# Kernel optimization log

Hardware: AMD Instinct MI355X
Metric: run time of the kernel (lower is better)

## Reference

```python
import jax, jax.numpy as jnp
import numpy as np

N = 100_000   # num_nodes
D = 64        # emb_dim
E = 1_600_000 # num edges (before self loops)
L = 3         # n_layers
NEG_SLOPE = 0.2


def setup_inputs() -> dict:
    key = jax.random.key(0)
    ks = jax.random.split(key, 6)
    edge_index = jax.random.randint(ks[0], (2, E), 0, N, dtype=jnp.int32)
    # xavier-ish init for embedding and per-layer GATConv params
    emb = jax.random.normal(ks[1], (N, D), jnp.float32) * (1.0 / np.sqrt(D))
    W = jax.random.normal(ks[2], (L, D, D), jnp.float32) * (1.0 / np.sqrt(D))
    att_src = jax.random.normal(ks[3], (L, D), jnp.float32) * 0.1
    att_dst = jax.random.normal(ks[4], (L, D), jnp.float32) * 0.1
    bias = jnp.zeros((L, D), jnp.float32)
    return {"edge_index": edge_index, "emb": emb, "W": W,
            "att_src": att_src, "att_dst": att_dst, "bias": bias}


def _gat_layer(x, src, dst, W, a_s, a_d, b):
    # PyG GATConv, heads=1, concat=False, self-loops already in (src, dst)
    h = x @ W                                   # [N, D]
    e_s = h @ a_s                               # [N] per-node src score
    e_d = h @ a_d                               # [N] per-node dst score
    e = jax.nn.leaky_relu(e_s[src] + e_d[dst], NEG_SLOPE)   # [E']
    # segment softmax grouped by destination node (max is detached in PyG)
    m = jax.lax.stop_gradient(jax.ops.segment_max(e, dst, num_segments=N))
    ex = jnp.exp(e - m[dst])
    denom = jax.ops.segment_sum(ex, dst, num_segments=N)
    alpha = ex / (denom[dst] + 1e-16)           # [E']
    out = jax.ops.segment_sum(alpha[:, None] * h[src], dst, num_segments=N)
    return out + b


def reference(edge_index, emb, W, att_src, att_dst, bias):
    loops = jnp.arange(N, dtype=edge_index.dtype)
    src = jnp.concatenate([edge_index[0], loops])
    dst = jnp.concatenate([edge_index[1], loops])
    x = emb
    outs = [x]
    for l in range(L):
        x = jax.nn.elu(_gat_layer(x, src, dst, W[l], att_src[l], att_dst[l], bias[l]))
        outs.append(x)
    return jnp.mean(jnp.stack(outs, axis=0), axis=0)  # [N, D]
```

## Files before the change

### kernel.cpp

```cpp
#include <hip/hip_runtime.h>
#include <hip/hip_bf16.h>


#define BSHIFT 9
#define NPB 512
#define COL_CAP 10240
#define FRAG_STRIDE 5120

typedef _Float16 v8h __attribute__((ext_vector_type(8)));
typedef float v4f __attribute__((ext_vector_type(4)));
typedef unsigned short u16x8 __attribute__((ext_vector_type(8)));

__device__ inline float bf2f(unsigned short u) {
    return __uint_as_float(((unsigned int)u) << 16);
}
__device__ inline unsigned short f2bf(float v) {
    __hip_bfloat16 b = __float2bfloat16(v);
    return *reinterpret_cast<unsigned short*>(&b);
}
__device__ inline unsigned short f2h_u(float v) {
    return __builtin_bit_cast(unsigned short, (_Float16)v);
}
__device__ inline float h2f_u(unsigned short u) {
    return (float)__builtin_bit_cast(_Float16, u);
}

__global__ __launch_bounds__(256) void detect_bf16_k(const unsigned int* raw, int* flag, int* ghist) {
    __shared__ int sc;
    if (threadIdx.x == 0) sc = 0;
    ghist[threadIdx.x] = 0;
    __syncthreads();
    int c = 0;
    for (int i = threadIdx.x; i < 4096; i += 256) {
        unsigned int b = (raw[i] >> 8) & 0x7Fu;
        if (b >= 0x3Bu && b <= 0x3Fu) c++;
    }
    atomicAdd(&sc, c);
    __syncthreads();
    if (threadIdx.x == 0) *flag = (sc > 2048) ? 1 : 0;
}

__device__ inline float load_in(const void* p, int i, int isbf) {
    if (isbf) return bf2f(((const unsigned short*)p)[i]);
    return ((const float*)p)[i];
}

__global__ __launch_bounds__(256) void conv_emb_k(const void* emb, unsigned short* x0,
                                                  int n, const int* flag) {
    int i = blockIdx.x * 256 + threadIdx.x;
    if (i >= n) return;
    x0[i] = f2h_u(load_in(emb, i, *flag));
}

__global__ __launch_bounds__(256) void conv_params_k(const void* W, const void* as_, const void* ad_,
                                                     const void* b_, unsigned short* Whf, float* bf,
                                                     int L_, const int* flag) {
    int i = blockIdx.x * 256 + threadIdx.x;
    int isbf = *flag;
    if (i < L_ * 4096) {
        int l = i >> 12, rem = i & 4095;
        int k = rem >> 6, c64 = rem & 63;
        int t = c64 >> 4, c = c64 & 15;
        int kf = k >> 5, quad = (k >> 3) & 3, j = k & 7;
        int f = t * 2 + kf, lane = quad * 16 + c;
        Whf[l * FRAG_STRIDE + (f * 64 + lane) * 8 + j] = f2h_u(load_in(W, i, isbf));
    }
    if (i < L_ * 1024) {
        int l = i >> 10, r = i & 1023;
        int kf = r >> 9, rr = r & 511;
        int lane = rr >> 3, j = rr & 7;
        int c = lane & 15, quad = lane >> 4;
        int k = kf * 32 + quad * 8 + j;
        float val = 0.f;
        if (c < 2) {
            const void* av = c ? ad_ : as_;
            float dot = 0.f;
            for (int cc = 0; cc < 64; ++cc)
                dot += load_in(W, l * 4096 + k * 64 + cc, isbf) * load_in(av, l * 64 + cc, isbf);
            val = dot;
        }
        Whf[l * FRAG_STRIDE + ((8 + kf) * 64 + lane) * 8 + j] = f2h_u(val);
    }
    if (i < L_ * 64) bf[i] = load_in(b_, i, isbf);
}


__global__ __launch_bounds__(256) void hist_k(const int* dst, int* ghist, int E) {
    __shared__ int h[256];
    h[threadIdx.x] = 0;
    __syncthreads();
    int cs = blockIdx.x * 4096;
    int ce = min(cs + 4096, E);
    for (int i = cs + threadIdx.x; i < ce; i += 256)
        atomicAdd(&h[dst[i] >> BSHIFT], 1);
    __syncthreads();
    if (h[threadIdx.x]) atomicAdd(&ghist[threadIdx.x], h[threadIdx.x]);
}

__global__ __launch_bounds__(256) void scan_nb_k(const int* ghist, int* pairs_base, int* col_base,
                                                 int* cursor, int* rowptr, int N, int E, int NB) {
    __shared__ int s1[256], s2[256];
    int t = threadIdx.x;
    int hv = (t < NB) ? ghist[t] : 0;
    int npb = (t < NB) ? min(N - (t << BSHIFT), NPB) : 0;
    s1[t] = hv; s2[t] = hv + npb;
    __syncthreads();
    for (int off = 1; off < 256; off <<= 1) {
        int t1 = (t >= off) ? s1[t - off] : 0;
        int t2 = (t >= off) ? s2[t - off] : 0;
        __syncthreads();
        s1[t] += t1; s2[t] += t2;
        __syncthreads();
    }
    if (t < NB) {
        pairs_base[t] = s1[t] - hv;
        cursor[t]     = s1[t] - hv;
        col_base[t]   = s2[t] - (hv + npb);
    }
    if (t == 0) rowptr[N] = E + N;
}

__global__ __launch_bounds__(256) void partition_k(const int* __restrict__ src,
                                                   const int* __restrict__ dst,
                                                   int* cursor, uint2* __restrict__ pairs,
                                                   int E, int NB) {
    __shared__ int cnt[256], base[256], rk[256];
    int t = threadIdx.x;
    cnt[t] = 0; rk[t] = 0;
    __syncthreads();
    int cs = blockIdx.x * 4096;
    int ce = min(cs + 4096, E);
    for (int i = cs + t; i < ce; i += 256)
        atomicAdd(&cnt[dst[i] >> BSHIFT], 1);
    __syncthreads();
    if (t < NB && cnt[t]) base[t] = atomicAdd(&cursor[t], cnt[t]);
    __syncthreads();
    for (int i = cs + t; i < ce; i += 256) {
        int d = dst[i];
        int b = d >> BSHIFT;
        int r = atomicAdd(&rk[b], 1);
        pairs[base[b] + r] = make_uint2((unsigned)src[i], (unsigned)d);
    }
}

__global__ __launch_bounds__(512) void build_k(const uint2* __restrict__ pairs,
                                               const int* __restrict__ ghist,
                                               const int* __restrict__ pairs_base,
                                               const int* __restrict__ col_base,
                                               int* __restrict__ rowptr, int* __restrict__ col,
                                               int N) {
    __shared__ int cnt[512], cnt2[512], sc[512], off[513];
    __shared__ int col_lds[COL_CAP];
    int b = blockIdx.x, t = threadIdx.x;
    int nloc = min(N - (b << BSHIFT), NPB);
    int ne = ghist[b], pb = pairs_base[b], cb = col_base[b];
    cnt[t] = 0; cnt2[t] = 0;
    __syncthreads();
    for (int i = t; i < ne; i += 512)
        atomicAdd(&cnt[pairs[pb + i].y & (NPB - 1)], 1);
    __syncthreads();
    int v = cnt[t] + (t < nloc ? 1 : 0);
    sc[t] = v;
    __syncthreads();
    for (int o = 1; o < 512; o <<= 1) {
        int tv = (t >= o) ? sc[t - o] : 0;
        __syncthreads();
        sc[t] += tv;
        __syncthreads();
    }
    off[t + 1] = sc[t];
    if (t == 0) off[0] = 0;
    __syncthreads();
    if (t < nloc) rowptr[(b << BSHIFT) + t] = cb + off[t];
    int total = off[nloc];
    bool fit = (total <= COL_CAP);
    for (int i = t; i < ne; i += 512) {
        uint2 p = pairs[pb + i];
        int loc = p.y & (NPB - 1);
        int pos = off[loc] + atomicAdd(&cnt2[loc], 1);
        if (fit) col_lds[pos] = (int)p.x;
        else     col[cb + pos] = (int)p.x;
    }
    if (t < nloc) {
        int pos = off[t + 1] - 1;
        int sv = (b << BSHIFT) + t;
        if (fit) col_lds[pos] = sv;
        else     col[cb + pos] = sv;
    }
    __syncthreads();
    if (fit)
        for (int i = t; i < total; i += 512) col[cb + i] = col_lds[i];
}


__global__ __launch_bounds__(256) void gemm_k(const unsigned short* __restrict__ x,
                                              const unsigned short* __restrict__ Whf,
                                              unsigned short* __restrict__ h,
                                              float* __restrict__ es, float* __restrict__ ed,
                                              int n, int nblk, int nwaves) {
    int lane = threadIdx.x & 63;
    int gwave = (blockIdx.x * 256 + threadIdx.x) >> 6;
    int c = lane & 15, quad = lane >> 4;

    v8h bfr[10];
    #pragma unroll
    for (int f = 0; f < 10; ++f)
        bfr[f] = *(const v8h*)(Whf + (size_t)(f * 64 + lane) * 8);

    v4f z = {0.f, 0.f, 0.f, 0.f};
    for (int nb = gwave; nb < nblk; nb += nwaves) {
        int base = nb * 16;
        int m = base + c; if (m >= n) m = n - 1;
        const v8h a0 = *(const v8h*)(x + (size_t)m * 64 + quad * 8);
        const v8h a1 = *(const v8h*)(x + (size_t)m * 64 + 32 + quad * 8);
        v4f acc[5];
        #pragma unroll
        for (int t = 0; t < 5; ++t) {
            acc[t] = __builtin_amdgcn_mfma_f32_16x16x32_f16(a0, bfr[2 * t], z, 0, 0, 0);
            acc[t] = __builtin_amdgcn_mfma_f32_16x16x32_f16(a1, bfr[2 * t + 1], acc[t], 0, 0, 0);
        }
        #pragma unroll
        for (int r = 0; r < 4; ++r) {
            int row = base + quad * 4 + r;
            if (row < n) {
                #pragma unroll
                for (int t = 0; t < 4; ++t)
                    h[(size_t)row * 64 + t * 16 + c] = f2h_u(acc[t][r]);
                if (c == 0) es[row] = acc[4][r];
                if (c == 1) ed[row] = acc[4][r];
            }
        }
    }
}

__device__ inline float elu_f(float v) { return v > 0.f ? v : (__expf(v) - 1.f); }

__global__ __launch_bounds__(256) void agg_k(const unsigned short* __restrict__ h,
                                             const float* __restrict__ es,
                                             const float* __restrict__ ed, const int* __restrict__ rowptr,
                                             const int* __restrict__ col, const float* __restrict__ bias,
                                             unsigned short* __restrict__ xo, int n) {
    int gw = (blockIdx.x * 256 + threadIdx.x) >> 6;
    int lane = threadIdx.x & 63;
    if (gw >= n) return;
    int start = rowptr[gw], end = rowptr[gw + 1];
    int deg = end - start;
    float edd = ed[gw];

    if (deg <= 64) {
        int c = 0;
        float e = -1e30f;
        if (lane < deg) {
            c = col[start + lane];
            float t = es[c] + edd;
            e = t > 0.f ? t : 0.2f * t;
        }
        float m = e;
        #pragma unroll
        for (int off = 32; off; off >>= 1) m = fmaxf(m, __shfl_xor(m, off));
        float ex = (lane < deg) ? __expf(e - m) : 0.f;
        float sum = ex;
        #pragma unroll
        for (int off = 32; off; off >>= 1) sum += __shfl_xor(sum, off);
        float a = ex / (sum + 1e-16f);

        int g = lane >> 3, j = lane & 7;
        float acc[8];
        #pragma unroll
        for (int i = 0; i < 8; ++i) acc[i] = 0.f;
        for (int t = 0; t < deg; t += 16) {
            int i0 = t + g, i1 = t + 8 + g;
            int   s0  = __shfl(c, i0), s1 = __shfl(c, i1);
            float al0 = __shfl(a, i0), al1 = __shfl(a, i1);
            bool p0 = i0 < deg, p1 = i1 < deg;
            u16x8 hv0, hv1;
            if (p0) hv0 = *(const u16x8*)(h + (size_t)s0 * 64 + j * 8);
            if (p1) hv1 = *(const u16x8*)(h + (size_t)s1 * 64 + j * 8);
            if (p0) {
                #pragma unroll
                for (int i = 0; i < 8; ++i) acc[i] = fmaf(al0, h2f_u(hv0[i]), acc[i]);
            }
            if (p1) {
                #pragma unroll
                for (int i = 0; i < 8; ++i) acc[i] = fmaf(al1, h2f_u(hv1[i]), acc[i]);
            }
        }
        #pragma unroll
        for (int off = 8; off < 64; off <<= 1)
            #pragma unroll
            for (int i = 0; i < 8; ++i)
                acc[i] += __shfl_xor(acc[i], off);

        if (g == 0) {
            u16x8 o;
            #pragma unroll
            for (int i = 0; i < 8; ++i)
                o[i] = f2h_u(elu_f(acc[i] + bias[j * 8 + i]));
            *(u16x8*)(xo + (size_t)gw * 64 + j * 8) = o;
        }
    } else {
        float m = -1e30f;
        for (int k = start + lane; k < end; k += 64) {
            float e = es[col[k]] + edd;
            e = e > 0.f ? e : 0.2f * e;
            m = fmaxf(m, e);
        }
        #pragma unroll
        for (int off = 32; off; off >>= 1) m = fmaxf(m, __shfl_xor(m, off));
        float sum = 0.f;
        for (int k = start + lane; k < end; k += 64) {
            float e = es[col[k]] + edd;
            e = e > 0.f ? e : 0.2f * e;
            sum += __expf(e - m);
        }
        #pragma unroll
        for (int off = 32; off; off >>= 1) sum += __shfl_xor(sum, off);
        float inv = 1.f / (sum + 1e-16f);
        float acc = 0.f;
        for (int k = start; k < end; ++k) {
            int s = col[k];
            float e = es[s] + edd;
            e = e > 0.f ? e : 0.2f * e;
            float al = __expf(e - m) * inv;
            acc = fmaf(al, h2f_u(h[(size_t)s * 64 + lane]), acc);
        }
        xo[(size_t)gw * 64 + lane] = f2h_u(elu_f(acc + bias[lane]));
    }
}

__global__ __launch_bounds__(256) void finalize_k(const unsigned short* __restrict__ x0,
                                                  const unsigned short* __restrict__ x1,
                                                  const unsigned short* __restrict__ x2,
                                                  const unsigned short* __restrict__ x3,
                                                  void* __restrict__ out, const int* flag, int n8) {
    int i = blockIdx.x * 256 + threadIdx.x;
    if (i >= n8) return;
    size_t base = (size_t)i * 8;
    u16x8 a = *(const u16x8*)(x0 + base);
    u16x8 b = *(const u16x8*)(x1 + base);
    u16x8 c = *(const u16x8*)(x2 + base);
    u16x8 d = *(const u16x8*)(x3 + base);
    float v[8];
    #pragma unroll
    for (int k = 0; k < 8; ++k)
        v[k] = (h2f_u(a[k]) + h2f_u(b[k]) + h2f_u(c[k]) + h2f_u(d[k])) * 0.25f;
    if (*flag) {
        u16x8 o;
        #pragma unroll
        for (int k = 0; k < 8; ++k) o[k] = f2bf(v[k]);
        *(u16x8*)((unsigned short*)out + base) = o;
    } else {
        float4 o0 = make_float4(v[0], v[1], v[2], v[3]);
        float4 o1 = make_float4(v[4], v[5], v[6], v[7]);
        *(float4*)((float*)out + base) = o0;
        *(float4*)((float*)out + base + 4) = o1;
    }
}


extern "C" void kernel_launch(void* const* d_in, const int* in_sizes, int n_in,
                              void* d_out, int out_size, void* d_ws, size_t ws_size,
                              hipStream_t stream) {
    const int*  edge = (const int*)d_in[0];
    const void* emb  = d_in[1];
    const void* W    = d_in[2];
    const void* as_  = d_in[3];
    const void* ad_  = d_in[4];
    const void* b_   = d_in[5];

    const int E = in_sizes[0] / 2;
    const int N = in_sizes[1] / 64;
    const int L = in_sizes[2] / 4096;
    const int NB = (N + NPB - 1) >> BSHIFT;
    const size_t N64 = (size_t)N * 64;

    char* p = (char*)d_ws;
    auto take = [&](size_t bytes) { char* r = p; p += (bytes + 255) & ~(size_t)255; return r; };
    unsigned short* x0 = (unsigned short*)take(N64 * 2);
    unsigned short* x1 = (unsigned short*)take(N64 * 2);
    unsigned short* x3 = (unsigned short*)take(N64 * 2);
    unsigned short* h  = (unsigned short*)take(N64 * 2);
    uint2* pairs   = (uint2*)take((size_t)E * 8 > N64 * 2 ? (size_t)E * 8 : N64 * 2);
    unsigned short* x2 = (unsigned short*)pairs;
    float* es      = (float*)take((size_t)N * 4);
    float* ed      = (float*)take((size_t)N * 4);
    unsigned short* Whf = (unsigned short*)take((size_t)L * FRAG_STRIDE * 2);
    float* bf      = (float*)take((size_t)L * 64 * 4);
    int* rowptr    = (int*)take((size_t)(N + 1) * 4);
    int* col       = (int*)take((size_t)(E + N) * 4);
    int* ghist     = (int*)take(256 * 4);
    int* pairs_base= (int*)take(256 * 4);
    int* col_base  = (int*)take(256 * 4);
    int* cursor    = (int*)take(256 * 4);
    int* flag      = (int*)take(4);

    const int* srcp = edge;
    const int* dstp = edge + E;
    int nchunk = (E + 4095) / 4096;

    detect_bf16_k<<<1, 256, 0, stream>>>((const unsigned int*)emb, flag, ghist);
    conv_emb_k<<<(int)((N64 + 255) / 256), 256, 0, stream>>>(emb, x0, (int)N64, flag);
    conv_params_k<<<(L * 4096 + 255) / 256, 256, 0, stream>>>(W, as_, ad_, b_, Whf, bf, L, flag);

    hist_k<<<nchunk, 256, 0, stream>>>(dstp, ghist, E);
    scan_nb_k<<<1, 256, 0, stream>>>(ghist, pairs_base, col_base, cursor, rowptr, N, E, NB);
    partition_k<<<nchunk, 256, 0, stream>>>(srcp, dstp, cursor, pairs, E, NB);
    build_k<<<NB, 512, 0, stream>>>(pairs, ghist, pairs_base, col_base, rowptr, col, N);

    const int nblk = (N + 15) / 16;
    const int ggrid = 512;
    unsigned short* xs[4] = {x0, x1, x2, x3};
    for (int l = 0; l < L; ++l) {
        gemm_k<<<ggrid, 256, 0, stream>>>(xs[l], Whf + (size_t)l * FRAG_STRIDE,
                                          h, es, ed, N, nblk, ggrid * 4);
        agg_k<<<(N + 3) / 4, 256, 0, stream>>>(h, es, ed, rowptr, col, bf + l * 64, xs[l + 1], N);
    }
    finalize_k<<<(int)((N64 / 8 + 255) / 256), 256, 0, stream>>>(x0, x1, x2, x3, d_out, flag,
                                                                 (int)(N64 / 8));
}
```

Before: 375.2 us.

## Fuse finalize into last aggregation, merge conversions, deterministic partition scan

Folds the layer-mean finalize into the last aggregation kernel so the final layer output is never written and reread. Merges the embedding and parameter conversion kernels into one launch. Replaces the atomic cursor partitioning with per-chunk histograms plus a per-bucket scan, so partition_k no longer recounts its chunk or issues global atomics. This adds one scan kernel and a histogram buffer that is read twice.

Measured after the change: 353.8 us. -5.7%, faster.

```diff
diff --git a/kernel.cpp b/kernel.cpp
--- a/kernel.cpp
+++ b/kernel.cpp
@@ -6,6 +6,7 @@
 #define NPB 512
 #define COL_CAP 10240
 #define FRAG_STRIDE 5120
+#define CHUNK 4096
 
 typedef _Float16 v8h __attribute__((ext_vector_type(8)));
 typedef float v4f __attribute__((ext_vector_type(4)));
@@ -25,10 +26,9 @@
     return (float)__builtin_bit_cast(_Float16, u);
 }
 
-__global__ __launch_bounds__(256) void detect_bf16_k(const unsigned int* raw, int* flag, int* ghist) {
+__global__ __launch_bounds__(256) void detect_bf16_k(const unsigned int* raw, int* flag) {
     __shared__ int sc;
     if (threadIdx.x == 0) sc = 0;
-    ghist[threadIdx.x] = 0;
     __syncthreads();
     int c = 0;
     for (int i = threadIdx.x; i < 4096; i += 256) {
@@ -45,18 +45,13 @@
     return ((const float*)p)[i];
 }
 
-__global__ __launch_bounds__(256) void conv_emb_k(const void* emb, unsigned short* x0,
-                                                  int n, const int* flag) {
-    int i = blockIdx.x * 256 + threadIdx.x;
-    if (i >= n) return;
-    x0[i] = f2h_u(load_in(emb, i, *flag));
-}
-
-__global__ __launch_bounds__(256) void conv_params_k(const void* W, const void* as_, const void* ad_,
-                                                     const void* b_, unsigned short* Whf, float* bf,
-                                                     int L_, const int* flag) {
+__global__ __launch_bounds__(256) void conv_k(const void* emb, const void* W, const void* as_,
+                                              const void* ad_, const void* b_, unsigned short* x0,
+                                              unsigned short* Whf, float* bf, int n, int L_,
+                                              const int* flag) {
     int i = blockIdx.x * 256 + threadIdx.x;
     int isbf = *flag;
+    if (i < n) x0[i] = f2h_u(load_in(emb, i, isbf));
     if (i < L_ * 4096) {
         int l = i >> 12, rem = i & 4095;
         int k = rem >> 6, c64 = rem & 63;
@@ -85,20 +80,43 @@
 }
 
 
-__global__ __launch_bounds__(256) void hist_k(const int* dst, int* ghist, int E) {
+__global__ __launch_bounds__(256) void hist_k(const int* __restrict__ dst, int* __restrict__ bh,
+                                              int E, int nchunk) {
     __shared__ int h[256];
     h[threadIdx.x] = 0;
     __syncthreads();
-    int cs = blockIdx.x * 4096;
-    int ce = min(cs + 4096, E);
+    int cs = blockIdx.x * CHUNK;
+    int ce = min(cs + CHUNK, E);
     for (int i = cs + threadIdx.x; i < ce; i += 256)
         atomicAdd(&h[dst[i] >> BSHIFT], 1);
     __syncthreads();
-    if (h[threadIdx.x]) atomicAdd(&ghist[threadIdx.x], h[threadIdx.x]);
+    bh[threadIdx.x * nchunk + blockIdx.x] = h[threadIdx.x];
+}
+
+__global__ __launch_bounds__(256) void scanb_k(int* __restrict__ bh, int* __restrict__ ghist,
+                                               int nchunk) {
+    __shared__ int s[256];
+    int b = blockIdx.x, t = threadIdx.x;
+    int i0 = 2 * t, i1 = 2 * t + 1;
+    int v0 = (i0 < nchunk) ? bh[b * nchunk + i0] : 0;
+    int v1 = (i1 < nchunk) ? bh[b * nchunk + i1] : 0;
+    int p = v0 + v1;
+    s[t] = p;
+    __syncthreads();
+    for (int off = 1; off < 256; off <<= 1) {
+        int tv = (t >= off) ? s[t - off] : 0;
+        __syncthreads();
+        s[t] += tv;
+        __syncthreads();
+    }
+    int excl = s[t] - p;
+    if (i0 < nchunk) bh[b * nchunk + i0] = excl;
+    if (i1 < nchunk) bh[b * nchunk + i1] = excl + v0;
+    if (t == 255) ghist[b] = s[255];
 }
 
 __global__ __launch_bounds__(256) void scan_nb_k(const int* ghist, int* pairs_base, int* col_base,
-                                                 int* cursor, int* rowptr, int N, int E, int NB) {
+                                                 int* rowptr, int N, int E, int NB) {
     __shared__ int s1[256], s2[256];
     int t = threadIdx.x;
     int hv = (t < NB) ? ghist[t] : 0;
@@ -114,7 +132,6 @@
     }
     if (t < NB) {
         pairs_base[t] = s1[t] - hv;
-        cursor[t]     = s1[t] - hv;
         col_base[t]   = s2[t] - (hv + npb);
     }
     if (t == 0) rowptr[N] = E + N;
@@ -122,19 +139,17 @@
 
 __global__ __launch_bounds__(256) void partition_k(const int* __restrict__ src,
                                                    const int* __restrict__ dst,
-                                                   int* cursor, uint2* __restrict__ pairs,
-                                                   int E, int NB) {
-    __shared__ int cnt[256], base[256], rk[256];
+                                                   const int* __restrict__ bh,
+                                                   const int* __restrict__ pairs_base,
+                                                   uint2* __restrict__ pairs,
+                                                   int E, int NB, int nchunk) {
+    __shared__ int base[256], rk[256];
     int t = threadIdx.x;
-    cnt[t] = 0; rk[t] = 0;
-    __syncthreads();
-    int cs = blockIdx.x * 4096;
-    int ce = min(cs + 4096, E);
-    for (int i = cs + t; i < ce; i += 256)
-        atomicAdd(&cnt[dst[i] >> BSHIFT], 1);
-    __syncthreads();
-    if (t < NB && cnt[t]) base[t] = atomicAdd(&cursor[t], cnt[t]);
-    __syncthreads();
+    base[t] = (t < NB) ? pairs_base[t] + bh[t * nchunk + blockIdx.x] : 0;
+    rk[t] = 0;
+    __syncthreads();
+    int cs = blockIdx.x * CHUNK;
+    int ce = min(cs + CHUNK, E);
     for (int i = cs + t; i < ce; i += 256) {
         int d = dst[i];
         int b = d >> BSHIFT;
@@ -239,7 +254,12 @@
                                              const float* __restrict__ es,
                                              const float* __restrict__ ed, const int* __restrict__ rowptr,
                                              const int* __restrict__ col, const float* __restrict__ bias,
-                                             unsigned short* __restrict__ xo, int n) {
+                                             unsigned short* __restrict__ xo,
+                                             const unsigned short* __restrict__ x0,
+                                             const unsigned short* __restrict__ x1,
+                                             const unsigned short* __restrict__ x2,
+                                             void* __restrict__ out, const int* __restrict__ flag,
+                                             int write_out, int n) {
     int gw = (blockIdx.x * 256 + threadIdx.x) >> 6;
     int lane = threadIdx.x & 63;
     if (gw >= n) return;
@@ -292,11 +312,36 @@
                 acc[i] += __shfl_xor(acc[i], off);
 
         if (g == 0) {
-            u16x8 o;
+            size_t base = (size_t)gw * 64 + j * 8;
+            float y[8];
             #pragma unroll
             for (int i = 0; i < 8; ++i)
-                o[i] = f2h_u(elu_f(acc[i] + bias[j * 8 + i]));
-            *(u16x8*)(xo + (size_t)gw * 64 + j * 8) = o;
+                y[i] = elu_f(acc[i] + bias[j * 8 + i]);
+            if (write_out) {
+                u16x8 a0v = *(const u16x8*)(x0 + base);
+                u16x8 a1v = *(const u16x8*)(x1 + base);
+                u16x8 a2v = *(const u16x8*)(x2 + base);
+                float v[8];
+                #pragma unroll
+                for (int i = 0; i < 8; ++i)
+                    v[i] = (h2f_u(a0v[i]) + h2f_u(a1v[i]) + h2f_u(a2v[i]) + y[i]) * 0.25f;
+                if (*flag) {
+                    u16x8 o;
+                    #pragma unroll
+                    for (int i = 0; i < 8; ++i) o[i] = f2bf(v[i]);
+                    *(u16x8*)((unsigned short*)out + base) = o;
+                } else {
+                    float4 o0 = make_float4(v[0], v[1], v[2], v[3]);
+                    float4 o1 = make_float4(v[4], v[5], v[6], v[7]);
+                    *(float4*)((float*)out + base) = o0;
+                    *(float4*)((float*)out + base + 4) = o1;
+                }
+            } else {
+                u16x8 o;
+                #pragma unroll
+                for (int i = 0; i < 8; ++i) o[i] = f2h_u(y[i]);
+                *(u16x8*)(xo + base) = o;
+            }
         }
     } else {
         float m = -1e30f;
@@ -324,36 +369,15 @@
             float al = __expf(e - m) * inv;
             acc = fmaf(al, h2f_u(h[(size_t)s * 64 + lane]), acc);
         }
-        xo[(size_t)gw * 64 + lane] = f2h_u(elu_f(acc + bias[lane]));
-    }
-}
-
-__global__ __launch_bounds__(256) void finalize_k(const unsigned short* __restrict__ x0,
-                                                  const unsigned short* __restrict__ x1,
-                                                  const unsigned short* __restrict__ x2,
-                                                  const unsigned short* __restrict__ x3,
-                                                  void* __restrict__ out, const int* flag, int n8) {
-    int i = blockIdx.x * 256 + threadIdx.x;
-    if (i >= n8) return;
-    size_t base = (size_t)i * 8;
-    u16x8 a = *(const u16x8*)(x0 + base);
-    u16x8 b = *(const u16x8*)(x1 + base);
-    u16x8 c = *(const u16x8*)(x2 + base);
-    u16x8 d = *(const u16x8*)(x3 + base);
-    float v[8];
-    #pragma unroll
-    for (int k = 0; k < 8; ++k)
-        v[k] = (h2f_u(a[k]) + h2f_u(b[k]) + h2f_u(c[k]) + h2f_u(d[k])) * 0.25f;
-    if (*flag) {
-        u16x8 o;
-        #pragma unroll
-        for (int k = 0; k < 8; ++k) o[k] = f2bf(v[k]);
-        *(u16x8*)((unsigned short*)out + base) = o;
-    } else {
-        float4 o0 = make_float4(v[0], v[1], v[2], v[3]);
-        float4 o1 = make_float4(v[4], v[5], v[6], v[7]);
-        *(float4*)((float*)out + base) = o0;
-        *(float4*)((float*)out + base + 4) = o1;
+        size_t base = (size_t)gw * 64 + lane;
+        float y = elu_f(acc + bias[lane]);
+        if (write_out) {
+            float v = (h2f_u(x0[base]) + h2f_u(x1[base]) + h2f_u(x2[base]) + y) * 0.25f;
+            if (*flag) ((unsigned short*)out)[base] = f2bf(v);
+            else       ((float*)out)[base] = v;
+        } else {
+            xo[base] = f2h_u(y);
+        }
     }
 }
 
@@ -372,6 +396,7 @@
     const int N = in_sizes[1] / 64;
     const int L = in_sizes[2] / 4096;
     const int NB = (N + NPB - 1) >> BSHIFT;
+    const int nchunk = (E + CHUNK - 1) / CHUNK;
     const size_t N64 = (size_t)N * 64;
 
     char* p = (char*)d_ws;
@@ -388,23 +413,23 @@
     float* bf      = (float*)take((size_t)L * 64 * 4);
     int* rowptr    = (int*)take((size_t)(N + 1) * 4);
     int* col       = (int*)take((size_t)(E + N) * 4);
+    int* bh        = (int*)take((size_t)256 * 512 * 4);
     int* ghist     = (int*)take(256 * 4);
     int* pairs_base= (int*)take(256 * 4);
     int* col_base  = (int*)take(256 * 4);
-    int* cursor    = (int*)take(256 * 4);
     int* flag      = (int*)take(4);
 
     const int* srcp = edge;
     const int* dstp = edge + E;
-    int nchunk = (E + 4095) / 4096;
-
-    detect_bf16_k<<<1, 256, 0, stream>>>((const unsigned int*)emb, flag, ghist);
-    conv_emb_k<<<(int)((N64 + 255) / 256), 256, 0, stream>>>(emb, x0, (int)N64, flag);
-    conv_params_k<<<(L * 4096 + 255) / 256, 256, 0, stream>>>(W, as_, ad_, b_, Whf, bf, L, flag);
-
-    hist_k<<<nchunk, 256, 0, stream>>>(dstp, ghist, E);
-    scan_nb_k<<<1, 256, 0, stream>>>(ghist, pairs_base, col_base, cursor, rowptr, N, E, NB);
-    partition_k<<<nchunk, 256, 0, stream>>>(srcp, dstp, cursor, pairs, E, NB);
+
+    detect_bf16_k<<<1, 256, 0, stream>>>((const unsigned int*)emb, flag);
+    conv_k<<<(int)((N64 + 255) / 256), 256, 0, stream>>>(emb, W, as_, ad_, b_, x0, Whf, bf,
+                                                         (int)N64, L, flag);
+
+    hist_k<<<nchunk, 256, 0, stream>>>(dstp, bh, E, nchunk);
+    scanb_k<<<NB, 256, 0, stream>>>(bh, ghist, nchunk);
+    scan_nb_k<<<1, 256, 0, stream>>>(ghist, pairs_base, col_base, rowptr, N, E, NB);
+    partition_k<<<nchunk, 256, 0, stream>>>(srcp, dstp, bh, pairs_base, pairs, E, NB, nchunk);
     build_k<<<NB, 512, 0, stream>>>(pairs, ghist, pairs_base, col_base, rowptr, col, N);
 
     const int nblk = (N + 15) / 16;
@@ -413,8 +438,8 @@
     for (int l = 0; l < L; ++l) {
         gemm_k<<<ggrid, 256, 0, stream>>>(xs[l], Whf + (size_t)l * FRAG_STRIDE,
                                           h, es, ed, N, nblk, ggrid * 4);
-        agg_k<<<(N + 3) / 4, 256, 0, stream>>>(h, es, ed, rowptr, col, bf + l * 64, xs[l + 1], N);
-    }
-    finalize_k<<<(int)((N64 / 8 + 255) / 256), 256, 0, stream>>>(x0, x1, x2, x3, d_out, flag,
-                                                                 (int)(N64 / 8));
-}
+        agg_k<<<(N + 3) / 4, 256, 0, stream>>>(h, es, ed, rowptr, col, bf + l * 64, xs[l + 1],
+                                               x0, x1, x2, d_out, flag,
+                                               (l == L - 1) ? 1 : 0, N);
+    }
+}
```
